# Performance work log

Hardware: AMD Instinct MI355X
Metric: run time of the kernel (lower is better)

The kernel has to match this reference:

```python
import jax, jax.numpy as jnp
import numpy as np

DIM = 64; N_C = 2000; N_P = 1500; N_ATOMS = 40; L_PROT = 512
N_FP = 10000; N_WORD = 8000; DIM_D = 1024; DIM_P = 1024
L_GNN = 3; L_CNN = 3; L_GCN = 2; WIN = 5; B = 4096


def setup_inputs() -> dict:
    key = jax.random.key(0)
    ks = jax.random.split(key, 32)
    g = lambda i, shape, s=0.05: jax.random.normal(ks[i], shape, dtype=jnp.float32) * s
    inp = {}
    inp["idx_c"] = jax.random.randint(ks[0], (B,), 0, N_C)
    inp["idx_p"] = jax.random.randint(ks[1], (B,), 0, N_P)
    inp["compounds"] = jax.random.randint(ks[2], (N_C, N_ATOMS), 0, N_FP)
    inp["proteins"] = jax.random.randint(ks[3], (N_P, L_PROT), 0, N_WORD)
    a = (jax.random.uniform(ks[4], (N_C, N_ATOMS, N_ATOMS)) < 0.1).astype(jnp.float32)
    inp["adjacencies"] = jnp.clip(a + jnp.swapaxes(a, 1, 2) + jnp.eye(N_ATOMS), 0.0, 1.0)
    ac = (jax.random.uniform(ks[5], (N_C, N_C)) < 0.005).astype(jnp.float32)
    inp["A_c"] = jnp.clip(ac + ac.T + jnp.eye(N_C), 0.0, 1.0) / 20.0
    ap = (jax.random.uniform(ks[6], (N_P, N_P)) < 0.005).astype(jnp.float32)
    inp["A_p"] = jnp.clip(ap + ap.T + jnp.eye(N_P), 0.0, 1.0) / 20.0
    inp["embed_fp"] = g(7, (N_FP, DIM), 1.0)
    inp["embed_word"] = g(8, (N_WORD, DIM), 1.0)
    inp["Xs_c"] = g(9, (N_C, DIM), 1.0)
    inp["Xs_p"] = g(10, (N_P, DIM), 1.0)
    inp["drug_feat"] = g(11, (N_C, DIM_D), 1.0)
    inp["protein_feat"] = g(12, (N_P, DIM_P), 1.0)
    inp["W_gnn"] = g(13, (L_GNN, DIM, DIM)); inp["b_gnn"] = jnp.zeros((L_GNN, DIM), jnp.float32)
    inp["K_cnn"] = g(14, (L_CNN, 2 * WIN + 1, 2 * WIN + 1)); inp["b_cnn"] = jnp.zeros((L_CNN,), jnp.float32)
    inp["W_gcn_d"] = g(15, (L_GCN, DIM, DIM)); inp["b_gcn_d"] = jnp.zeros((L_GCN, DIM), jnp.float32)
    inp["W_gcn_p"] = g(16, (L_GCN, DIM, DIM)); inp["b_gcn_p"] = jnp.zeros((L_GCN, DIM), jnp.float32)
    inp["Wd1"] = g(17, (DIM_D, 2 * DIM)); inp["bd1"] = jnp.zeros((2 * DIM,), jnp.float32)
    inp["Wd2"] = g(18, (2 * DIM, DIM)); inp["bd2"] = jnp.zeros((DIM,), jnp.float32)
    inp["Wd3"] = g(19, (DIM, DIM)); inp["bd3"] = jnp.zeros((DIM,), jnp.float32)
    inp["Wp1"] = g(20, (DIM_P, 2 * DIM)); inp["bp1"] = jnp.zeros((2 * DIM,), jnp.float32)
    inp["Wp2"] = g(21, (2 * DIM, DIM)); inp["bp2"] = jnp.zeros((DIM,), jnp.float32)
    inp["Wp3"] = g(22, (DIM, DIM)); inp["bp3"] = jnp.zeros((DIM,), jnp.float32)
    inp["Wo1"] = g(23, (6 * DIM, 4 * DIM)); inp["bo1"] = jnp.zeros((4 * DIM,), jnp.float32)
    inp["Wo2"] = g(24, (4 * DIM, 4 * DIM)); inp["bo2"] = jnp.zeros((4 * DIM,), jnp.float32)
    inp["Wo3"] = g(25, (4 * DIM, 4 * DIM)); inp["bo3"] = jnp.zeros((4 * DIM,), jnp.float32)
    inp["W_int"] = g(26, (4 * DIM, 2)); inp["b_int"] = jnp.zeros((2,), jnp.float32)
    return inp


def reference(idx_c, idx_p, compounds, proteins, adjacencies, A_c, A_p,
              embed_fp, embed_word, Xs_c, Xs_p, drug_feat, protein_feat,
              W_gnn, b_gnn, K_cnn, b_cnn, W_gcn_d, b_gcn_d, W_gcn_p, b_gcn_p,
              Wd1, bd1, Wd2, bd2, Wd3, bd3, Wp1, bp1, Wp2, bp2, Wp3, bp3,
              Wo1, bo1, Wo2, bo2, Wo3, bo3, W_int, b_int):
    # ---- intrinsic compound embedding: batched GNN over all compounds.
    # (travInvolve's BFS selects a superset of idx_c; computing all rows is
    #  output-equivalent since only Xs_c_int[idx_c] is consumed.)
    xs = embed_fp[compounds]                                  # [N_c, A, d]
    for i in range(L_GNN):
        hs = jax.nn.relu(jnp.einsum('nad,de->nae', xs, W_gnn[i]) + b_gnn[i])
        xs = xs + jnp.einsum('nab,nbd->nad', adjacencies, hs)
    comp_int = jnp.mean(xs, axis=1)                           # [N_c, d]

    # ---- intrinsic protein embedding: batched single-channel 2D CNN (SAME pad)
    x = embed_word[proteins][:, None]                         # [N_p, 1, L, d]
    for i in range(L_CNN):
        x = jax.nn.relu(jax.lax.conv_general_dilated(
            x, K_cnn[i][None, None], (1, 1), [(WIN, WIN), (WIN, WIN)]) + b_cnn[i])
    prot_int = jnp.mean(x[:, 0], axis=1)                      # mean over length -> [N_p, d]

    # ---- relational GCN diffusion over global adjacency
    Xc = Xs_c
    for i in range(L_GCN):
        Xc = jax.nn.relu((A_c @ Xc) @ W_gcn_d[i] + b_gcn_d[i])
    Xp = Xs_p
    for i in range(L_GCN):
        Xp = jax.nn.relu((A_p @ Xp) @ W_gcn_p[i] + b_gcn_p[i])

    # ---- annotation MLPs
    fd = jax.nn.relu(drug_feat[idx_c] @ Wd1 + bd1)
    fd = jax.nn.relu(fd @ Wd2 + bd2)
    fd = jax.nn.relu(fd @ Wd3 + bd3)
    fp = jax.nn.relu(protein_feat[idx_p] @ Wp1 + bp1)
    fp = jax.nn.relu(fp @ Wp2 + bp2)
    fp = jax.nn.relu(fp @ Wp3 + bp3)

    cat = jnp.concatenate([comp_int[idx_c], Xc[idx_c], fd,
                           prot_int[idx_p], Xp[idx_p], fp], axis=1)  # [B, 6d]
    h = jax.nn.relu(cat @ Wo1 + bo1)
    h = jax.nn.relu(h @ Wo2 + bo2)
    h = jax.nn.relu(h @ Wo3 + bo3)
    return jax.nn.sigmoid(h @ W_int + b_int)                  # [B, 2]
```

## Files before the change

### kernel.cpp

```cpp
#include <hip/hip_runtime.h>
#include <math.h>

#define NC 2000
#define NP 1500
#define NA 40
#define LP 512
#define BSZ 4096
#define NW 8000
#define KPC 2048
#define KPP 1536

typedef _Float16 half8_t __attribute__((ext_vector_type(8)));
typedef _Float16 half4_t __attribute__((ext_vector_type(4)));
typedef float f32x4 __attribute__((ext_vector_type(4)));

struct CnnS { half8_t bufA8[62 * 16]; half8_t bufB8[62 * 16]; };
struct GnnS { _Float16 xs[48 * 72]; _Float16 hsT[64 * 72]; };
struct MlpS { float cb[4][16][17]; };
struct EpiS { float Ys[64][68]; float Ws[64][64]; };

__device__ __forceinline__ int swz_off(int row, int half_col)
{
    int b = half_col >> 3;
    return row * 128 + (((b & 8) | ((b ^ row) & 7)) << 3) + (half_col & 7);
}

__global__ void prep_all(
    const float* __restrict__ K_cnn, _Float16* __restrict__ wtab,
    const float* __restrict__ ew, _Float16* __restrict__ ehp,
    const float* __restrict__ df, const float* __restrict__ pf,
    const float* __restrict__ wd1, const float* __restrict__ wd2, const float* __restrict__ wd3,
    const float* __restrict__ wp1, const float* __restrict__ wp2, const float* __restrict__ wp3,
    const float* __restrict__ wo1, const float* __restrict__ wo2, const float* __restrict__ wo3,
    _Float16* __restrict__ dfh, _Float16* __restrict__ pfh,
    _Float16* __restrict__ wd1t, _Float16* __restrict__ wd2t, _Float16* __restrict__ wd3t,
    _Float16* __restrict__ wp1t, _Float16* __restrict__ wp2t, _Float16* __restrict__ wp3t,
    _Float16* __restrict__ wo1t, _Float16* __restrict__ wo2t, _Float16* __restrict__ wo3t,
    const float* __restrict__ wgnn, _Float16* __restrict__ wgt,
    const float* __restrict__ Ac, const float* __restrict__ Ap,
    const float* __restrict__ Xc, const float* __restrict__ Xp,
    _Float16* __restrict__ Ahc, _Float16* __restrict__ Ahp,
    _Float16* __restrict__ Xtc, _Float16* __restrict__ Xtp,
    _Float16* __restrict__ Xtca, _Float16* __restrict__ Xtpa)
{
    int j = blockIdx.x * 256 + threadIdx.x;
    if (j < 16896) {
        int L = j / 5632, rem = j % 5632;
        int dr = rem >> 9, r2 = rem & 511, ln = r2 >> 3, i = r2 & 7;
        int dc = 8 * (ln >> 4) + i - (ln & 15);
        float v = (dc >= 0 && dc < 11) ? K_cnn[L * 121 + dr * 11 + dc] : 0.f;
        wtab[j] = (_Float16)v;
        return;
    }
    j -= 16896;
    if (j < NW * 80) {
        int w = j / 80, h = j - w * 80;
        float v = (h >= 13 && h < 77) ? ew[w * 64 + (h - 13)] : 0.f;
        ehp[j] = (_Float16)v;
        return;
    }
    j -= NW * 80;
    if (j < 2048000) { dfh[j] = (_Float16)df[j]; return; }
    j -= 2048000;
    if (j < 1536000) { pfh[j] = (_Float16)pf[j]; return; }
    j -= 1536000;
    if (j < 131072) { int n = j >> 10, k = j & 1023; wd1t[j] = (_Float16)wd1[k * 128 + n]; return; }
    j -= 131072;
    if (j < 8192)  { int n = j >> 7, k = j & 127; wd2t[j] = (_Float16)wd2[k * 64 + n]; return; }
    j -= 8192;
    if (j < 4096)  { int n = j >> 6, k = j & 63; wd3t[j] = (_Float16)wd3[k * 64 + n]; return; }
    j -= 4096;
    if (j < 131072) { int n = j >> 10, k = j & 1023; wp1t[j] = (_Float16)wp1[k * 128 + n]; return; }
    j -= 131072;
    if (j < 8192)  { int n = j >> 7, k = j & 127; wp2t[j] = (_Float16)wp2[k * 64 + n]; return; }
    j -= 8192;
    if (j < 4096)  { int n = j >> 6, k = j & 63; wp3t[j] = (_Float16)wp3[k * 64 + n]; return; }
    j -= 4096;
    if (j < 98304) { int n = j / 384, k = j - n * 384; wo1t[j] = (_Float16)wo1[k * 256 + n]; return; }
    j -= 98304;
    if (j < 65536) { int n = j >> 8, k = j & 255; wo2t[j] = (_Float16)wo2[k * 256 + n]; return; }
    j -= 65536;
    if (j < 65536) { int n = j >> 8, k = j & 255; wo3t[j] = (_Float16)wo3[k * 256 + n]; return; }
    j -= 65536;
    if (j < 12288) { int l = j >> 12, rem = j & 4095, nn = rem >> 6, k = rem & 63;
                     wgt[j] = (_Float16)wgnn[l * 4096 + k * 64 + nn]; return; }
    j -= 12288;
    if (j < KPC * KPC) {
        int r = j >> 11, c = j & (KPC - 1);
        Ahc[j] = (_Float16)((r < NC && c < NC) ? Ac[(size_t)r * NC + c] : 0.f);
        return;
    }
    j -= KPC * KPC;
    if (j < KPP * KPP) {
        int r = j / KPP, c = j - r * KPP;
        Ahp[j] = (_Float16)((r < NP && c < NP) ? Ap[(size_t)r * NP + c] : 0.f);
        return;
    }
    j -= KPP * KPP;
    if (j < 64 * KPC) {
        int c = j >> 11, r = j & (KPC - 1);
        Xtc[j] = (_Float16)((r < NC) ? Xc[(size_t)r * 64 + c] : 0.f);
        return;
    }
    j -= 64 * KPC;
    if (j < 64 * KPP) {
        int c = j / KPP, r = j - c * KPP;
        Xtp[j] = (_Float16)((r < NP) ? Xp[(size_t)r * 64 + c] : 0.f);
        return;
    }
    j -= 64 * KPP;
    if (j < 64 * KPC) { Xtca[j] = (_Float16)0.f; return; }
    j -= 64 * KPC;
    if (j < 64 * KPP) { Xtpa[j] = (_Float16)0.f; }
}
#define PREP_TOTAL (16896 + NW * 80 + 2048000 + 1536000 + 131072 + 8192 + 4096 + 131072 + 8192 + 4096 + 98304 + 65536 + 65536 + 12288 + KPC * KPC + KPP * KPP + 64 * KPC + 64 * KPP + 64 * KPC + 64 * KPP)

__device__ __forceinline__ void gnn_body(GnnS& G, int n,
    const int* __restrict__ compounds, const float* __restrict__ adjacencies,
    const float* __restrict__ embed_fp, const _Float16* __restrict__ wgt,
    const float* __restrict__ b_gnn, _Float16* __restrict__ comp_h)
{
    const int tid = threadIdx.x, lane = tid & 63, wid = tid >> 6;
    const int m = lane & 15, g = lane >> 4;
    const int colL = wid * 16 + m;

    for (int j = tid; j < 48 * 64; j += 256) {
        int r = j >> 6, c = j & 63;
        _Float16 v = (_Float16)0.f;
        if (r < 40) v = (_Float16)embed_fp[(size_t)compounds[n * NA + r] * 64 + c];
        G.xs[r * 72 + c] = v;
    }
    for (int j = tid; j < 64 * 72 / 8; j += 256) ((half8_t*)G.hsT)[j] = (half8_t){};

    half8_t adjf[3][2];
    #pragma unroll
    for (int t = 0; t < 3; ++t)
        #pragma unroll
        for (int s = 0; s < 2; ++s) {
            half8_t v = {};
            int row = t * 16 + m, k0 = s * 32 + 8 * g;
            if (row < 40 && k0 < 40) {
                const float* src = &adjacencies[(size_t)n * 1600 + row * 40 + k0];
                #pragma unroll
                for (int i = 0; i < 8; ++i) v[i] = (_Float16)src[i];
            }
            adjf[t][s] = v;
        }
    __syncthreads();

    for (int l = 0; l < 3; ++l) {
        float bcol = b_gnn[l * 64 + colL];
        #pragma unroll
        for (int t = 0; t < 3; ++t) {
            f32x4 acc = {bcol, bcol, bcol, bcol};
            #pragma unroll
            for (int s = 0; s < 2; ++s) {
                half8_t a = *(const half8_t*)&G.xs[(t * 16 + m) * 72 + s * 32 + 8 * g];
                half8_t b = *(const half8_t*)&wgt[(size_t)(l * 64 + colL) * 64 + s * 32 + 8 * g];
                acc = __builtin_amdgcn_mfma_f32_16x16x32_f16(a, b, acc, 0, 0, 0);
            }
            half4_t h4;
            #pragma unroll
            for (int j = 0; j < 4; ++j) h4[j] = (_Float16)fmaxf(acc[j], 0.f);
            *(half4_t*)&G.hsT[colL * 72 + t * 16 + 4 * g] = h4;
        }
        __syncthreads();
        #pragma unroll
        for (int t = 0; t < 3; ++t) {
            f32x4 acc;
            #pragma unroll
            for (int j = 0; j < 4; ++j)
                acc[j] = (float)G.xs[(t * 16 + 4 * g + j) * 72 + colL];
            #pragma unroll
            for (int s = 0; s < 2; ++s) {
                half8_t b = *(const half8_t*)&G.hsT[colL * 72 + s * 32 + 8 * g];
                acc = __builtin_amdgcn_mfma_f32_16x16x32_f16(adjf[t][s], b, acc, 0, 0, 0);
            }
            #pragma unroll
            for (int j = 0; j < 4; ++j)
                G.xs[(t * 16 + 4 * g + j) * 72 + colL] = (_Float16)acc[j];
        }
        __syncthreads();
    }
    if (tid < 64) {
        float s = 0.f;
        for (int r = 0; r < 40; ++r) s += (float)G.xs[r * 72 + tid];
        comp_h[n * 64 + tid] = (_Float16)(s * (1.0f / 40.0f));
    }
}

__device__ __forceinline__ void cnn_body(CnnS& S, int cb_,
    const int* __restrict__ proteins, const _Float16* __restrict__ ehp,
    const half8_t* __restrict__ wtab, const float* __restrict__ b_cnn,
    float* __restrict__ prot_part)
{
    _Float16* bufA = (_Float16*)S.bufA8;
    _Float16* bufB = (_Float16*)S.bufB8;
    half8_t* bufA8 = S.bufA8;
    half8_t* bufB8 = S.bufB8;
    const int tid = threadIdx.x, lane = tid & 63, wid = tid >> 6;
    const int tile = cb_ & 15, p = cb_ >> 4;
    const int t0 = tile * 32;
    const int c0 = wid * 16;
    const int m = lane & 15, g = lane >> 4;

    half8_t z = {};
    for (int e = tid; e < 62 * 9; e += 256) {
        int i = e / 9, a = 1 + (e - 9 * i);
        int gr = t0 - 15 + i;
        half8_t v = z;
        if (gr >= 0 && gr < LP)
            v = *(const half8_t*)&ehp[(size_t)proteins[p * LP + gr] * 80 + 8 * a];
        *(half8_t*)&bufA[i * 128 + (((a & 8) | ((a ^ i) & 7)) << 3)] = v;
    }
    for (int e = tid; e < 62 * 4; e += 256) {
        int i = e >> 2, w = e & 3;
        if (w == 0)      bufA8[i * 16 + (8 | ((10 ^ i) & 7))] = z;
        else if (w == 1) bufB8[i * 16 + ((1 ^ i) & 7)] = z;
        else {
            int blk = 7 + w;
            bufB8[i * 16 + ((blk & 8) | ((blk ^ i) & 7))] = z;
        }
    }

    half8_t wf[11];
    auto load_wf = [&](int L) {
        #pragma unroll
        for (int dr = 0; dr < 11; ++dr) wf[dr] = wtab[L * 11 * 64 + dr * 64 + lane];
    };
    auto conv_tile = [&](const _Float16* src, int r0, float bias) -> f32x4 {
        f32x4 acc = {bias, bias, bias, bias};
        const int B0 = (c0 + 8) >> 3;
        #pragma unroll
        for (int dr = 0; dr < 11; ++dr) {
            int R = r0 - 5 + dr + m;
            int b = B0 + g;
            half8_t a = *(const half8_t*)&src[R * 128 + (((b & 8) | ((b ^ R) & 7)) << 3)];
            acc = __builtin_amdgcn_mfma_f32_16x16x32_f16(a, wf[dr], acc, 0, 0, 0);
        }
        return acc;
    };
    auto store_tile = [&](_Float16* dst, int r0, f32x4 acc) {
        int pc = c0 + 13 + m;
        #pragma unroll
        for (int j = 0; j < 4; ++j) {
            int row = r0 + 4 * g + j;
            int og = t0 - 15 + row;
            float v = fmaxf(acc[j], 0.f);
            dst[swz_off(row, pc)] = (_Float16)((og >= 0 && og < LP) ? v : 0.f);
        }
    };

    load_wf(0);
    __syncthreads();
    {
        float b0 = b_cnn[0];
        const int r0s[4] = {5, 21, 37, 41};
        #pragma unroll
        for (int k = 0; k < 4; ++k) store_tile(bufB, r0s[k], conv_tile(bufA, r0s[k], b0));
    }
    __syncthreads();
    load_wf(1);
    {
        float b1 = b_cnn[1];
        const int r0s[3] = {10, 26, 36};
        #pragma unroll
        for (int k = 0; k < 3; ++k) store_tile(bufA, r0s[k], conv_tile(bufB, r0s[k], b1));
    }
    __syncthreads();
    load_wf(2);
    {
        float b2 = b_cnn[2];
        float cs = 0.f;
        const int r0s[2] = {15, 31};
        #pragma unroll
        for (int k = 0; k < 2; ++k) {
            f32x4 acc = conv_tile(bufA, r0s[k], b2);
            #pragma unroll
            for (int j = 0; j < 4; ++j) cs += fmaxf(acc[j], 0.f);
        }
        cs += __shfl_xor(cs, 16, 64);
        cs += __shfl_xor(cs, 32, 64);
        if (lane < 16)
            prot_part[((size_t)p * 16 + tile) * 64 + c0 + lane] = cs;
    }
}

__device__ __forceinline__ void spk_body(int x, int y,
    const _Float16* __restrict__ Ah, const _Float16* __restrict__ Xt,
    float* __restrict__ part, int M, int Kp)
{
    const int tid = threadIdx.x, wid = tid >> 6, lane = tid & 63;
    const int m = lane & 15, g = lane >> 4;
    const int row0 = x * 64 + wid * 16;
    const int chunk = Kp >> 3, k0 = y * chunk;
    const _Float16* Apr = Ah + (size_t)(row0 + m) * Kp + 8 * g;
    f32x4 acc[4] = {};
    for (int kb = k0; kb < k0 + chunk; kb += 32) {
        half8_t af = *(const half8_t*)&Apr[kb];
        #pragma unroll
        for (int t = 0; t < 4; ++t) {
            half8_t bf = *(const half8_t*)&Xt[(size_t)(t * 16 + m) * Kp + kb + 8 * g];
            acc[t] = __builtin_amdgcn_mfma_f32_16x16x32_f16(af, bf, acc[t], 0, 0, 0);
        }
    }
    #pragma unroll
    for (int t = 0; t < 4; ++t)
        #pragma unroll
        for (int j = 0; j < 4; ++j) {
            int row = row0 + 4 * g + j;
            if (row < M) part[((size_t)y * M + row) * 64 + t * 16 + m] = acc[t][j];
        }
}

__device__ __forceinline__ void epi_body(EpiS& S, int x,
    const float* __restrict__ part, int M, const float* __restrict__ W,
    const float* __restrict__ bias, _Float16* __restrict__ H,
    _Float16* __restrict__ XtN, int Kp)
{
    const int rb = x * 64;
    const int tid = threadIdx.x;
    for (int j = tid; j < 4096; j += 256) S.Ws[j >> 6][j & 63] = W[j];
    for (int j = tid; j < 4096; j += 256) {
        int r = j >> 6, c = j & 63;
        float sum = 0.f;
        if (rb + r < M)
            for (int t = 0; t < 8; ++t) sum += part[((size_t)t * M + rb + r) * 64 + c];
        S.Ys[r][c] = sum;
    }
    __syncthreads();
    const int tx = tid & 15, ty = tid >> 4;
    float acc[4][4];
    #pragma unroll
    for (int i = 0; i < 4; ++i)
        #pragma unroll
        for (int j = 0; j < 4; ++j) acc[i][j] = bias[tx * 4 + j];
    for (int d = 0; d < 64; ++d) {
        float a0 = S.Ys[ty * 4 + 0][d], a1 = S.Ys[ty * 4 + 1][d];
        float a2 = S.Ys[ty * 4 + 2][d], a3 = S.Ys[ty * 4 + 3][d];
        float4 w4 = *(const float4*)&S.Ws[d][tx * 4];
        acc[0][0] += a0 * w4.x; acc[0][1] += a0 * w4.y; acc[0][2] += a0 * w4.z; acc[0][3] += a0 * w4.w;
        acc[1][0] += a1 * w4.x; acc[1][1] += a1 * w4.y; acc[1][2] += a1 * w4.z; acc[1][3] += a1 * w4.w;
        acc[2][0] += a2 * w4.x; acc[2][1] += a2 * w4.y; acc[2][2] += a2 * w4.z; acc[2][3] += a2 * w4.w;
        acc[3][0] += a3 * w4.x; acc[3][1] += a3 * w4.y; acc[3][2] += a3 * w4.z; acc[3][3] += a3 * w4.w;
    }
    #pragma unroll
    for (int i = 0; i < 4; ++i) {
        int row = rb + ty * 4 + i;
        if (row < M) {
            #pragma unroll
            for (int j = 0; j < 4; ++j) {
                int col = tx * 4 + j;
                float v = fmaxf(acc[i][j], 0.f);
                if (H)   H[(size_t)row * 64 + col] = (_Float16)v;
                if (XtN) XtN[(size_t)col * Kp + row] = (_Float16)v;
            }
        }
    }
}

template<int NT, bool GATHER>
__device__ __forceinline__ void mlp_body(MlpS& S, int x, int y,
    const _Float16* __restrict__ A, const int* __restrict__ idx,
    const _Float16* __restrict__ Bt, const float* __restrict__ bias,
    _Float16* __restrict__ C, int K, int N)
{
    const int tid = threadIdx.x, wid = tid >> 6, lane = tid & 63;
    const int m = lane & 15, g = lane >> 4;
    const int row0 = x * 64 + wid * 16;
    const int col0 = y * (NT * 16);
    size_t arow = GATHER ? (size_t)idx[row0 + m] : (size_t)(row0 + m);
    const _Float16* Ap = A + arow * (size_t)K + 8 * g;
    f32x4 acc[NT] = {};
    for (int kb = 0; kb < K; kb += 32) {
        half8_t af = *(const half8_t*)&Ap[kb];
        #pragma unroll
        for (int t = 0; t < NT; ++t) {
            half8_t bf = *(const half8_t*)&Bt[(size_t)(col0 + t * 16 + m) * K + kb + 8 * g];
            acc[t] = __builtin_amdgcn_mfma_f32_16x16x32_f16(af, bf, acc[t], 0, 0, 0);
        }
    }
    const int rr = lane >> 2, c4 = (lane & 3) * 4;
    #pragma unroll
    for (int t = 0; t < NT; ++t) {
        #pragma unroll
        for (int j = 0; j < 4; ++j) S.cb[wid][4 * g + j][m] = acc[t][j];
        half4_t h;
        #pragma unroll
        for (int j = 0; j < 4; ++j)
            h[j] = (_Float16)fmaxf(S.cb[wid][rr][c4 + j] + bias[col0 + t * 16 + c4 + j], 0.f);
        *(half4_t*)&C[(size_t)(row0 + rr) * N + col0 + t * 16 + c4] = h;
    }
}

#define MEGA_CNN0 NC
#define MEGA_SPK0 (NC + 16 * NP)
#define MEGA_MLP0 (MEGA_SPK0 + 512)
#define MEGA_TOTAL (MEGA_MLP0 + 512)

__global__ __launch_bounds__(256) void mega_kernel(
    const int* __restrict__ proteins, const _Float16* __restrict__ ehp,
    const half8_t* __restrict__ wtab, const float* __restrict__ b_cnn,
    float* __restrict__ prot_part,
    const int* __restrict__ compounds, const float* __restrict__ adjacencies,
    const float* __restrict__ embed_fp, const _Float16* __restrict__ wgt,
    const float* __restrict__ b_gnn, _Float16* __restrict__ comp_h,
    const _Float16* __restrict__ Ah_c, const _Float16* __restrict__ Xt_c, float* __restrict__ part_c,
    const _Float16* __restrict__ Ah_p, const _Float16* __restrict__ Xt_p, float* __restrict__ part_p,
    const _Float16* __restrict__ drug_h, const int* __restrict__ idx_c,
    const _Float16* __restrict__ wd1t, const float* __restrict__ bd1, _Float16* __restrict__ fd1h,
    const _Float16* __restrict__ protf_h, const int* __restrict__ idx_p,
    const _Float16* __restrict__ wp1t, const float* __restrict__ bp1, _Float16* __restrict__ fp1h)
{
    __shared__ union { CnnS c; GnnS g; MlpS m; } sm;
    const int bx = blockIdx.x;

    if (bx >= MEGA_MLP0) {
        int idx = bx - MEGA_MLP0;
        int z = idx >> 8, rem = idx & 255, y = rem >> 6, x = rem & 63;
        if (z == 0) mlp_body<2, true>(sm.m, x, y, drug_h, idx_c, wd1t, bd1, fd1h, 1024, 128);
        else        mlp_body<2, true>(sm.m, x, y, protf_h, idx_p, wp1t, bp1, fp1h, 1024, 128);
        return;
    }
    if (bx >= MEGA_SPK0) {
        int idx = bx - MEGA_SPK0;
        int z = idx >> 8, rem = idx & 255, y = rem >> 5, x = rem & 31;
        if (z == 0)      spk_body(x, y, Ah_c, Xt_c, part_c, NC, KPC);
        else if (x < 24) spk_body(x, y, Ah_p, Xt_p, part_p, NP, KPP);
        return;
    }
    if (bx < MEGA_CNN0) {
        gnn_body(sm.g, bx, compounds, adjacencies, embed_fp, wgt, b_gnn, comp_h);
        return;
    }
    cnn_body(sm.c, bx - MEGA_CNN0, proteins, ehp, wtab, b_cnn, prot_part);
}

__global__ __launch_bounds__(256) void tail1(
    const float* __restrict__ prot_part, _Float16* __restrict__ prot_h,
    const float* __restrict__ part_c, const float* __restrict__ W_gcn_d, const float* __restrict__ b_gcn_d,
    _Float16* __restrict__ Xt_ca,
    const float* __restrict__ part_p, const float* __restrict__ W_gcn_p, const float* __restrict__ b_gcn_p,
    _Float16* __restrict__ Xt_pa,
    const _Float16* __restrict__ fd1h, const _Float16* __restrict__ wd2t, const float* __restrict__ bd2,
    _Float16* __restrict__ fd2h,
    const _Float16* __restrict__ fp1h, const _Float16* __restrict__ wp2t, const float* __restrict__ bp2,
    _Float16* __restrict__ fp2h)
{
    __shared__ union { EpiS e; MlpS m; } sm;
    int bx = blockIdx.x;
    const int tid = threadIdx.x;
    if (bx < 375) {
        int p = bx * 4 + (tid >> 6), c = tid & 63;
        float s = 0.f;
        for (int t = 0; t < 16; ++t) s += prot_part[((size_t)p * 16 + t) * 64 + c];
        prot_h[p * 64 + c] = (_Float16)(s * (1.0f / 512.0f));
        return;
    }
    bx -= 375;
    if (bx < 64) {
        int z = bx >> 5, x = bx & 31;
        if (z == 0)      epi_body(sm.e, x, part_c, NC, W_gcn_d, b_gcn_d, nullptr, Xt_ca, KPC);
        else if (x < 24) epi_body(sm.e, x, part_p, NP, W_gcn_p, b_gcn_p, nullptr, Xt_pa, KPP);
        return;
    }
    bx -= 64;
    {
        int z = bx >> 8, rem = bx & 255, y = rem >> 6, x = rem & 63;
        if (z == 0) mlp_body<1, false>(sm.m, x, y, fd1h, nullptr, wd2t, bd2, fd2h, 128, 64);
        else        mlp_body<1, false>(sm.m, x, y, fp1h, nullptr, wp2t, bp2, fp2h, 128, 64);
    }
}

__global__ __launch_bounds__(256) void tail2(
    const _Float16* __restrict__ Ah_c, const _Float16* __restrict__ Xt_ca, float* __restrict__ part_c,
    const _Float16* __restrict__ Ah_p, const _Float16* __restrict__ Xt_pa, float* __restrict__ part_p,
    const _Float16* __restrict__ fd2h, const _Float16* __restrict__ wd3t, const float* __restrict__ bd3,
    _Float16* __restrict__ fd3h,
    const _Float16* __restrict__ fp2h, const _Float16* __restrict__ wp3t, const float* __restrict__ bp3,
    _Float16* __restrict__ fp3h)
{
    __shared__ MlpS sm;
    int bx = blockIdx.x;
    if (bx < 512) {
        int z = bx >> 8, rem = bx & 255, y = rem >> 5, x = rem & 31;
        if (z == 0)      spk_body(x, y, Ah_c, Xt_ca, part_c, NC, KPC);
        else if (x < 24) spk_body(x, y, Ah_p, Xt_pa, part_p, NP, KPP);
        return;
    }
    bx -= 512;
    {
        int z = bx >> 8, rem = bx & 255, y = rem >> 6, x = rem & 63;
        if (z == 0) mlp_body<1, false>(sm, x, y, fd2h, nullptr, wd3t, bd3, fd3h, 64, 64);
        else        mlp_body<1, false>(sm, x, y, fp2h, nullptr, wp3t, bp3, fp3h, 64, 64);
    }
}

__global__ __launch_bounds__(256) void epi2_kernel(
    const float* __restrict__ part_c, const float* __restrict__ W0, const float* __restrict__ b0,
    _Float16* __restrict__ Xcb_h,
    const float* __restrict__ part_p, const float* __restrict__ W1, const float* __restrict__ b1,
    _Float16* __restrict__ Xpb_h)
{
    __shared__ EpiS sm;
    int bx = blockIdx.x;
    int z = bx >> 5, x = bx & 31;
    if (z == 0)      epi_body(sm, x, part_c, NC, W0, b0, Xcb_h, nullptr, KPC);
    else if (x < 24) epi_body(sm, x, part_p, NP, W1, b1, Xpb_h, nullptr, KPP);
}

__global__ __launch_bounds__(256) void mfma_head1(
    const int* __restrict__ idx_c, const int* __restrict__ idx_p,
    const _Float16* __restrict__ ci, const _Float16* __restrict__ xc, const _Float16* __restrict__ fd,
    const _Float16* __restrict__ pi, const _Float16* __restrict__ xp, const _Float16* __restrict__ fp,
    const _Float16* __restrict__ Bt, const float* __restrict__ bias, _Float16* __restrict__ C)
{
    const int tid = threadIdx.x, wid = tid >> 6, lane = tid & 63;
    const int m = lane & 15, g = lane >> 4;
    const int row0 = blockIdx.x * 64 + wid * 16;
    const int col0 = blockIdx.y * 32;
    int ic = idx_c[row0 + m], ip = idx_p[row0 + m];
    const _Float16* segs[6] = {
        ci + (size_t)ic * 64 + 8 * g,  xc + (size_t)ic * 64 + 8 * g,
        fd + (size_t)(row0 + m) * 64 + 8 * g,
        pi + (size_t)ip * 64 + 8 * g,  xp + (size_t)ip * 64 + 8 * g,
        fp + (size_t)(row0 + m) * 64 + 8 * g };
    f32x4 acc[2] = {};
    #pragma unroll
    for (int kb = 0; kb < 384; kb += 32) {
        half8_t af = *(const half8_t*)&segs[kb / 64][kb & 63];
        #pragma unroll
        for (int t = 0; t < 2; ++t) {
            half8_t bf = *(const half8_t*)&Bt[(size_t)(col0 + t * 16 + m) * 384 + kb + 8 * g];
            acc[t] = __builtin_amdgcn_mfma_f32_16x16x32_f16(af, bf, acc[t], 0, 0, 0);
        }
    }
    __shared__ MlpS sm;
    const int rr = lane >> 2, c4 = (lane & 3) * 4;
    #pragma unroll
    for (int t = 0; t < 2; ++t) {
        #pragma unroll
        for (int j = 0; j < 4; ++j) sm.cb[wid][4 * g + j][m] = acc[t][j];
        half4_t h;
        #pragma unroll
        for (int j = 0; j < 4; ++j)
            h[j] = (_Float16)fmaxf(sm.cb[wid][rr][c4 + j] + bias[col0 + t * 16 + c4 + j], 0.f);
        *(half4_t*)&C[(size_t)(row0 + rr) * 256 + col0 + t * 16 + c4] = h;
    }
}

__global__ __launch_bounds__(256) void mfma_head2(
    const _Float16* __restrict__ A, const _Float16* __restrict__ Bt,
    const float* __restrict__ bias, _Float16* __restrict__ C)
{
    __shared__ MlpS sm;
    mlp_body<2, false>(sm, blockIdx.x, blockIdx.y, A, nullptr, Bt, bias, C, 256, 256);
}

__global__ __launch_bounds__(256) void mfma_head3(
    const _Float16* __restrict__ A, const _Float16* __restrict__ Bt,
    const float* __restrict__ bias, const float* __restrict__ Wi, const float* __restrict__ bi,
    float* __restrict__ out)
{
    const int tid = threadIdx.x, wid = tid >> 6, lane = tid & 63;
    const int m = lane & 15, g = lane >> 4;
    const int row0 = blockIdx.x * 64 + wid * 16;
    const _Float16* Ap = A + (size_t)(row0 + m) * 256 + 8 * g;
    f32x4 acc[16] = {};
    for (int kb = 0; kb < 256; kb += 32) {
        half8_t af = *(const half8_t*)&Ap[kb];
        #pragma unroll
        for (int t = 0; t < 16; ++t) {
            half8_t bf = *(const half8_t*)&Bt[(size_t)(t * 16 + m) * 256 + kb + 8 * g];
            acc[t] = __builtin_amdgcn_mfma_f32_16x16x32_f16(af, bf, acc[t], 0, 0, 0);
        }
    }
    float p0[4] = {}, p1[4] = {};
    #pragma unroll
    for (int t = 0; t < 16; ++t) {
        float w0 = Wi[(t * 16 + m) * 2], w1 = Wi[(t * 16 + m) * 2 + 1];
        float bc = bias[t * 16 + m];
        #pragma unroll
        for (int j = 0; j < 4; ++j) {
            float v = fmaxf(acc[t][j] + bc, 0.f);
            p0[j] += v * w0; p1[j] += v * w1;
        }
    }
    #pragma unroll
    for (int d = 1; d < 16; d <<= 1) {
        #pragma unroll
        for (int j = 0; j < 4; ++j) {
            p0[j] += __shfl_xor(p0[j], d, 64);
            p1[j] += __shfl_xor(p1[j], d, 64);
        }
    }
    if (m == 0) {
        float B0 = bi[0], B1 = bi[1];
        #pragma unroll
        for (int j = 0; j < 4; ++j) {
            int r = row0 + 4 * g + j;
            out[r * 2 + 0] = 1.f / (1.f + expf(-(p0[j] + B0)));
            out[r * 2 + 1] = 1.f / (1.f + expf(-(p1[j] + B1)));
        }
    }
}

extern "C" void kernel_launch(void* const* d_in, const int* in_sizes, int n_in,
                              void* d_out, int out_size, void* d_ws, size_t ws_size,
                              hipStream_t stream)
{
    const int*   idx_c        = (const int*)  d_in[0];
    const int*   idx_p        = (const int*)  d_in[1];
    const int*   compounds    = (const int*)  d_in[2];
    const int*   proteins     = (const int*)  d_in[3];
    const float* adjacencies  = (const float*)d_in[4];
    const float* A_c          = (const float*)d_in[5];
    const float* A_p          = (const float*)d_in[6];
    const float* embed_fp     = (const float*)d_in[7];
    const float* embed_word   = (const float*)d_in[8];
    const float* Xs_c         = (const float*)d_in[9];
    const float* Xs_p         = (const float*)d_in[10];
    const float* drug_feat    = (const float*)d_in[11];
    const float* protein_feat = (const float*)d_in[12];
    const float* W_gnn        = (const float*)d_in[13];
    const float* b_gnn        = (const float*)d_in[14];
    const float* K_cnn        = (const float*)d_in[15];
    const float* b_cnn        = (const float*)d_in[16];
    const float* W_gcn_d      = (const float*)d_in[17];
    const float* b_gcn_d      = (const float*)d_in[18];
    const float* W_gcn_p      = (const float*)d_in[19];
    const float* b_gcn_p      = (const float*)d_in[20];
    const float* Wd1 = (const float*)d_in[21]; const float* bd1 = (const float*)d_in[22];
    const float* Wd2 = (const float*)d_in[23]; const float* bd2 = (const float*)d_in[24];
    const float* Wd3 = (const float*)d_in[25]; const float* bd3 = (const float*)d_in[26];
    const float* Wp1 = (const float*)d_in[27]; const float* bp1 = (const float*)d_in[28];
    const float* Wp2 = (const float*)d_in[29]; const float* bp2 = (const float*)d_in[30];
    const float* Wp3 = (const float*)d_in[31]; const float* bp3 = (const float*)d_in[32];
    const float* Wo1 = (const float*)d_in[33]; const float* bo1 = (const float*)d_in[34];
    const float* Wo2 = (const float*)d_in[35]; const float* bo2 = (const float*)d_in[36];
    const float* Wo3 = (const float*)d_in[37]; const float* bo3 = (const float*)d_in[38];
    const float* W_int = (const float*)d_in[39]; const float* b_int = (const float*)d_in[40];

    float* ws = (float*)d_ws;
    float* prot_part = ws; ws += NP * 16 * 64;
    float* wtab_g    = ws; ws += 8448;
    float* ehp_g     = ws; ws += NW * 40;
    float* part_c    = ws; ws += 8 * NC * 64;
    float* part_p    = ws; ws += 8 * NP * 64;
    _Float16* Ah_c  = (_Float16*)ws; ws += KPC * KPC / 2;
    _Float16* Ah_p  = (_Float16*)ws; ws += KPP * KPP / 2;
    _Float16* Xt_c  = (_Float16*)ws; ws += 32 * KPC;
    _Float16* Xt_p  = (_Float16*)ws; ws += 32 * KPP;
    _Float16* Xt_ca = (_Float16*)ws; ws += 32 * KPC;
    _Float16* Xt_pa = (_Float16*)ws; ws += 32 * KPP;
    _Float16* wgt_g = (_Float16*)ws; ws += 6144;
    _Float16* comp_h  = (_Float16*)ws; ws += NC * 32;
    _Float16* prot_h  = (_Float16*)ws; ws += NP * 32;
    _Float16* Xcb_h   = (_Float16*)ws; ws += NC * 32;
    _Float16* Xpb_h   = (_Float16*)ws; ws += NP * 32;
    _Float16* drug_h  = (_Float16*)ws; ws += NC * 512;
    _Float16* protf_h = (_Float16*)ws; ws += NP * 512;
    _Float16* wd1t = (_Float16*)ws; ws += 65536;
    _Float16* wd2t = (_Float16*)ws; ws += 4096;
    _Float16* wd3t = (_Float16*)ws; ws += 2048;
    _Float16* wp1t = (_Float16*)ws; ws += 65536;
    _Float16* wp2t = (_Float16*)ws; ws += 4096;
    _Float16* wp3t = (_Float16*)ws; ws += 2048;
    _Float16* wo1t = (_Float16*)ws; ws += 49152;
    _Float16* wo2t = (_Float16*)ws; ws += 32768;
    _Float16* wo3t = (_Float16*)ws; ws += 32768;
    _Float16* fd1h = (_Float16*)ws; ws += BSZ * 64;
    _Float16* fd2h = (_Float16*)ws; ws += BSZ * 32;
    _Float16* fd3h = (_Float16*)ws; ws += BSZ * 32;
    _Float16* fp1h = (_Float16*)ws; ws += BSZ * 64;
    _Float16* fp2h = (_Float16*)ws; ws += BSZ * 32;
    _Float16* fp3h = (_Float16*)ws; ws += BSZ * 32;
    _Float16* h1h  = (_Float16*)ws; ws += BSZ * 128;
    _Float16* h2h  = (_Float16*)ws; ws += BSZ * 128;
    (void)ws_size; (void)in_sizes; (void)n_in; (void)out_size;

    prep_all<<<(PREP_TOTAL + 255) / 256, 256, 0, stream>>>(
        K_cnn, (_Float16*)wtab_g, embed_word, (_Float16*)ehp_g,
        drug_feat, protein_feat, Wd1, Wd2, Wd3, Wp1, Wp2, Wp3, Wo1, Wo2, Wo3,
        drug_h, protf_h, wd1t, wd2t, wd3t, wp1t, wp2t, wp3t, wo1t, wo2t, wo3t,
        W_gnn, wgt_g,
        A_c, A_p, Xs_c, Xs_p, Ah_c, Ah_p, Xt_c, Xt_p, Xt_ca, Xt_pa);
    mega_kernel<<<MEGA_TOTAL, 256, 0, stream>>>(
        proteins, (const _Float16*)ehp_g, (const half8_t*)wtab_g, b_cnn, prot_part,
        compounds, adjacencies, embed_fp, wgt_g, b_gnn, comp_h,
        Ah_c, Xt_c, part_c, Ah_p, Xt_p, part_p,
        drug_h, idx_c, wd1t, bd1, fd1h, protf_h, idx_p, wp1t, bp1, fp1h);
    tail1<<<375 + 64 + 512, 256, 0, stream>>>(
        prot_part, prot_h,
        part_c, W_gcn_d, b_gcn_d, Xt_ca, part_p, W_gcn_p, b_gcn_p, Xt_pa,
        fd1h, wd2t, bd2, fd2h, fp1h, wp2t, bp2, fp2h);
    tail2<<<512 + 512, 256, 0, stream>>>(
        Ah_c, Xt_ca, part_c, Ah_p, Xt_pa, part_p,
        fd2h, wd3t, bd3, fd3h, fp2h, wp3t, bp3, fp3h);
    epi2_kernel<<<64, 256, 0, stream>>>(
        part_c, W_gcn_d + 4096, b_gcn_d + 64, Xcb_h,
        part_p, W_gcn_p + 4096, b_gcn_p + 64, Xpb_h);
    mfma_head1<<<dim3(64, 8), 256, 0, stream>>>(idx_c, idx_p, comp_h, Xcb_h, fd3h,
                                                prot_h, Xpb_h, fp3h, wo1t, bo1, h1h);
    mfma_head2<<<dim3(64, 8), 256, 0, stream>>>(h1h, wo2t, bo2, h2h);
    mfma_head3<<<64, 256, 0, stream>>>(h2h, wo3t, bo3, W_int, b_int, (float*)d_out);
}
```

Before: 365.4 us.

## Split mega kernel into GNN/CNN launch and separate SpMM/MLP launch

Moves the first GCN sparse-matmul and first MLP layer blocks out of the GNN/CNN mega kernel into a new launch, together with the protein mean reduction. The mega kernel's shared-memory union shrinks to the CNN/GNN structures only, which may raise occupancy. The cost is one more kernel launch and the loss of overlap between those independent stages inside a single grid.

```diff
diff --git a/kernel.cpp b/kernel.cpp
--- a/kernel.cpp
+++ b/kernel.cpp
@@ -393,18 +393,25 @@
     }
 }
 
-#define MEGA_CNN0 NC
-#define MEGA_SPK0 (NC + 16 * NP)
-#define MEGA_MLP0 (MEGA_SPK0 + 512)
-#define MEGA_TOTAL (MEGA_MLP0 + 512)
-
 __global__ __launch_bounds__(256) void mega_kernel(
     const int* __restrict__ proteins, const _Float16* __restrict__ ehp,
     const half8_t* __restrict__ wtab, const float* __restrict__ b_cnn,
     float* __restrict__ prot_part,
     const int* __restrict__ compounds, const float* __restrict__ adjacencies,
     const float* __restrict__ embed_fp, const _Float16* __restrict__ wgt,
-    const float* __restrict__ b_gnn, _Float16* __restrict__ comp_h,
+    const float* __restrict__ b_gnn, _Float16* __restrict__ comp_h)
+{
+    __shared__ union { CnnS c; GnnS g; } sm;
+    const int bx = blockIdx.x;
+    if (bx < NC) {
+        gnn_body(sm.g, bx, compounds, adjacencies, embed_fp, wgt, b_gnn, comp_h);
+        return;
+    }
+    cnn_body(sm.c, bx - NC, proteins, ehp, wtab, b_cnn, prot_part);
+}
+
+__global__ __launch_bounds__(256) void par1(
+    const float* __restrict__ prot_part, _Float16* __restrict__ prot_h,
     const _Float16* __restrict__ Ah_c, const _Float16* __restrict__ Xt_c, float* __restrict__ part_c,
     const _Float16* __restrict__ Ah_p, const _Float16* __restrict__ Xt_p, float* __restrict__ part_p,
     const _Float16* __restrict__ drug_h, const int* __restrict__ idx_c,
@@ -412,32 +419,32 @@
     const _Float16* __restrict__ protf_h, const int* __restrict__ idx_p,
     const _Float16* __restrict__ wp1t, const float* __restrict__ bp1, _Float16* __restrict__ fp1h)
 {
-    __shared__ union { CnnS c; GnnS g; MlpS m; } sm;
-    const int bx = blockIdx.x;
-
-    if (bx >= MEGA_MLP0) {
-        int idx = bx - MEGA_MLP0;
-        int z = idx >> 8, rem = idx & 255, y = rem >> 6, x = rem & 63;
-        if (z == 0) mlp_body<2, true>(sm.m, x, y, drug_h, idx_c, wd1t, bd1, fd1h, 1024, 128);
-        else        mlp_body<2, true>(sm.m, x, y, protf_h, idx_p, wp1t, bp1, fp1h, 1024, 128);
-        return;
-    }
-    if (bx >= MEGA_SPK0) {
-        int idx = bx - MEGA_SPK0;
-        int z = idx >> 8, rem = idx & 255, y = rem >> 5, x = rem & 31;
+    __shared__ MlpS sm;
+    int bx = blockIdx.x;
+    const int tid = threadIdx.x;
+    if (bx < 375) {
+        int p = bx * 4 + (tid >> 6), c = tid & 63;
+        float s = 0.f;
+        for (int t = 0; t < 16; ++t) s += prot_part[((size_t)p * 16 + t) * 64 + c];
+        prot_h[p * 64 + c] = (_Float16)(s * (1.0f / 512.0f));
+        return;
+    }
+    bx -= 375;
+    if (bx < 512) {
+        int z = bx >> 8, rem = bx & 255, y = rem >> 5, x = rem & 31;
         if (z == 0)      spk_body(x, y, Ah_c, Xt_c, part_c, NC, KPC);
         else if (x < 24) spk_body(x, y, Ah_p, Xt_p, part_p, NP, KPP);
         return;
     }
-    if (bx < MEGA_CNN0) {
-        gnn_body(sm.g, bx, compounds, adjacencies, embed_fp, wgt, b_gnn, comp_h);
-        return;
-    }
-    cnn_body(sm.c, bx - MEGA_CNN0, proteins, ehp, wtab, b_cnn, prot_part);
-}
-
-__global__ __launch_bounds__(256) void tail1(
-    const float* __restrict__ prot_part, _Float16* __restrict__ prot_h,
+    bx -= 512;
+    {
+        int z = bx >> 8, rem = bx & 255, y = rem >> 6, x = rem & 63;
+        if (z == 0) mlp_body<2, true>(sm, x, y, drug_h, idx_c, wd1t, bd1, fd1h, 1024, 128);
+        else        mlp_body<2, true>(sm, x, y, protf_h, idx_p, wp1t, bp1, fp1h, 1024, 128);
+    }
+}
+
+__global__ __launch_bounds__(256) void par2(
     const float* __restrict__ part_c, const float* __restrict__ W_gcn_d, const float* __restrict__ b_gcn_d,
     _Float16* __restrict__ Xt_ca,
     const float* __restrict__ part_p, const float* __restrict__ W_gcn_p, const float* __restrict__ b_gcn_p,
@@ -449,15 +456,6 @@
 {
     __shared__ union { EpiS e; MlpS m; } sm;
     int bx = blockIdx.x;
-    const int tid = threadIdx.x;
-    if (bx < 375) {
-        int p = bx * 4 + (tid >> 6), c = tid & 63;
-        float s = 0.f;
-        for (int t = 0; t < 16; ++t) s += prot_part[((size_t)p * 16 + t) * 64 + c];
-        prot_h[p * 64 + c] = (_Float16)(s * (1.0f / 512.0f));
-        return;
-    }
-    bx -= 375;
     if (bx < 64) {
         int z = bx >> 5, x = bx & 31;
         if (z == 0)      epi_body(sm.e, x, part_c, NC, W_gcn_d, b_gcn_d, nullptr, Xt_ca, KPC);
@@ -472,7 +470,7 @@
     }
 }
 
-__global__ __launch_bounds__(256) void tail2(
+__global__ __launch_bounds__(256) void par3(
     const _Float16* __restrict__ Ah_c, const _Float16* __restrict__ Xt_ca, float* __restrict__ part_c,
     const _Float16* __restrict__ Ah_p, const _Float16* __restrict__ Xt_pa, float* __restrict__ part_p,
     const _Float16* __restrict__ fd2h, const _Float16* __restrict__ wd3t, const float* __restrict__ bd3,
@@ -685,16 +683,17 @@
         drug_h, protf_h, wd1t, wd2t, wd3t, wp1t, wp2t, wp3t, wo1t, wo2t, wo3t,
         W_gnn, wgt_g,
         A_c, A_p, Xs_c, Xs_p, Ah_c, Ah_p, Xt_c, Xt_p, Xt_ca, Xt_pa);
-    mega_kernel<<<MEGA_TOTAL, 256, 0, stream>>>(
+    mega_kernel<<<NC + 16 * NP, 256, 0, stream>>>(
         proteins, (const _Float16*)ehp_g, (const half8_t*)wtab_g, b_cnn, prot_part,
-        compounds, adjacencies, embed_fp, wgt_g, b_gnn, comp_h,
+        compounds, adjacencies, embed_fp, wgt_g, b_gnn, comp_h);
+    par1<<<375 + 512 + 512, 256, 0, stream>>>(
+        prot_part, prot_h,
         Ah_c, Xt_c, part_c, Ah_p, Xt_p, part_p,
         drug_h, idx_c, wd1t, bd1, fd1h, protf_h, idx_p, wp1t, bp1, fp1h);
-    tail1<<<375 + 64 + 512, 256, 0, stream>>>(
-        prot_part, prot_h,
+    par2<<<64 + 512, 256, 0, stream>>>(
         part_c, W_gcn_d, b_gcn_d, Xt_ca, part_p, W_gcn_p, b_gcn_p, Xt_pa,
         fd1h, wd2t, bd2, fd2h, fp1h, wp2t, bp2, fp2h);
-    tail2<<<512 + 512, 256, 0, stream>>>(
+    par3<<<512 + 512, 256, 0, stream>>>(
         Ah_c, Xt_ca, part_c, Ah_p, Xt_pa, part_p,
         fd2h, wd3t, bd3, fd3h, fp2h, wp3t, bp3, fp3h);
     epi2_kernel<<<64, 256, 0, stream>>>(
```

New measurement: 341.5 us. 6.5% less time.
